# Performance work log

Measured on AMD Instinct MI355X. Metric: run time of the kernel, lower is better.

The kernel has to match this reference:

```python
import jax, jax.numpy as jnp
import numpy as np

B, C, L = 16, 128, 2048


def setup_inputs() -> dict:
    key = jax.random.key(0)
    ks = jax.random.split(key, 7)
    s = 1.0 / np.sqrt(C)  # torch Conv1d default init scale
    x = jax.random.normal(ks[0], (B, C, L), dtype=jnp.float32)
    W1 = jax.random.uniform(ks[1], (C, C), jnp.float32, -s, s)
    b1 = jax.random.uniform(ks[2], (C,), jnp.float32, -s, s)
    W2 = jax.random.uniform(ks[3], (C, C), jnp.float32, -s, s)
    b2 = jax.random.uniform(ks[4], (C,), jnp.float32, -s, s)
    W3 = jax.random.uniform(ks[5], (C, C), jnp.float32, -s, s)
    b3 = jax.random.uniform(ks[6], (C,), jnp.float32, -s, s)
    return {"x": x, "W1": W1, "b1": b1, "W2": W2, "b2": b2, "W3": W3, "b3": b3}


def _conv1x1(x, W, b):
    # x: [B,C,L], W: [out,in] -> [B,out,L]
    return jnp.einsum('oc,bcl->bol', W, x) + b[None, :, None]


def reference(x, W1, b1, W2, b2, W3, b3):
    q = _conv1x1(x, W1, b1).transpose(0, 2, 1)  # [B,L,C]
    k = _conv1x1(x, W2, b2).transpose(0, 2, 1)  # [B,L,C]
    v = _conv1x1(x, W3, b3).transpose(0, 2, 1)  # [B,L,C]
    attn = jnp.einsum('bic,bjc->bij', q, k)     # [B,L,L]
    attn = jax.nn.softmax(attn, axis=-1)
    out = jnp.einsum('bij,bjc->bic', attn, v)   # [B,L,C]
    return out.transpose(0, 2, 1)               # [B,C,L]
```

## Files before the change

### kernel.cpp

```cpp
#include <hip/hip_runtime.h>
#include <hip/hip_bf16.h>
#include <stdint.h>

#define B_ 16
#define C_ 128
#define L_ 2048
#define LOG2E 1.4426950408889634f

typedef __attribute__((ext_vector_type(8))) short bf16x8;
typedef __attribute__((ext_vector_type(4))) float f32x4;
typedef __attribute__((ext_vector_type(16))) float f32x16;
typedef __attribute__((ext_vector_type(4))) unsigned int u32x4;

typedef __attribute__((address_space(3))) unsigned int lds_u32_t;
typedef const __attribute__((address_space(1))) unsigned int gbl_u32_t;

__device__ __forceinline__ void gload_lds16(const void* g, void* l) {
  __builtin_amdgcn_global_load_lds((gbl_u32_t*)g,
                                   (lds_u32_t*)(unsigned long long)l, 16, 0, 0);
}

__device__ __forceinline__ unsigned short f2bf(float x) {
  union { float f; unsigned u; } v; v.f = x;
  unsigned u = v.u;
  u += 0x7fffu + ((u >> 16) & 1u);
  return (unsigned short)(u >> 16);
}

__device__ __forceinline__ unsigned pk2(float a, float b) {
  return (unsigned)f2bf(a) | ((unsigned)f2bf(b) << 16);
}

__device__ __forceinline__ unsigned cvtpk_bf16(float lo, float hi_) {
  unsigned r;
  asm("v_cvt_pk_bf16_f32 %0, %1, %2" : "=v"(r) : "v"(lo), "v"(hi_));
  return r;
}

__device__ __forceinline__ float max3f(float a, float b, float c) {
  float r;
  asm("v_max3_f32 %0, %1, %2, %3" : "=v"(r) : "v"(a), "v"(b), "v"(c));
  return r;
}

__device__ __forceinline__ f32x16 z16() {
  f32x16 v;
#pragma unroll
  for (int i = 0; i < 16; ++i) v[i] = 0.f;
  return v;
}

__device__ __forceinline__ float tmax16(const f32x16& v) {
  float m0 = max3f(v[0], v[1], v[2]);
  float m1 = max3f(v[3], v[4], v[5]);
  float m2_ = max3f(v[6], v[7], v[8]);
  float m3 = max3f(v[9], v[10], v[11]);
  float m4 = max3f(v[12], v[13], v[14]);
  float a = max3f(m0, m1, m2_);
  float b = max3f(m3, m4, v[15]);
  return fmaxf(a, b);
}

__device__ __forceinline__ float tsum16(const f32x16& v) {
  float a0 = v[0] + v[1],  a1 = v[2] + v[3];
  float a2 = v[4] + v[5],  a3 = v[6] + v[7];
  float a4 = v[8] + v[9],  a5 = v[10] + v[11];
  float a6 = v[12] + v[13], a7 = v[14] + v[15];
  float b0 = a0 + a1, b1 = a2 + a3, b2 = a4 + a5, b3 = a6 + a7;
  return (b0 + b1) + (b2 + b3);
}

__global__ __launch_bounds__(256, 2) void proj_kernel(
    const float* __restrict__ x,
    const float* __restrict__ W1, const float* __restrict__ b1,
    const float* __restrict__ W2, const float* __restrict__ b2,
    const float* __restrict__ W3, const float* __restrict__ b3,
    unsigned short* __restrict__ Qo, unsigned short* __restrict__ Ko,
    unsigned short* __restrict__ Vt)
{
  __shared__ unsigned short Xt[64][136];
  __shared__ unsigned short Wl[128][136];

  const int b  = blockIdx.x & 15;
  const int lt = blockIdx.x >> 4;
  const int l0 = lt * 64;
  const int tid = threadIdx.x;
  const int w = tid >> 6, lane = tid & 63, li = lane & 15, lg = lane >> 4;

  for (int it = 0; it < 8; ++it) {
    int idx = tid + it * 256;
    int c = idx >> 4, f4 = idx & 15;
    const float4 vv = *(const float4*)(x + (size_t)(b * C_ + c) * L_ + l0 + f4 * 4);
    Xt[f4 * 4 + 0][c] = f2bf(vv.x);
    Xt[f4 * 4 + 1][c] = f2bf(vv.y);
    Xt[f4 * 4 + 2][c] = f2bf(vv.z);
    Xt[f4 * 4 + 3][c] = f2bf(vv.w);
  }

  auto stageW = [&](const float* W) {
    for (int it = 0; it < 16; ++it) {
      int idx = tid + it * 256;
      int o = idx >> 5, f4 = idx & 31;
      const float4 vv = *(const float4*)(W + (size_t)o * C_ + f4 * 4);
      unsigned short* p = &Wl[o][f4 * 4];
      p[0] = f2bf(vv.x); p[1] = f2bf(vv.y); p[2] = f2bf(vv.z); p[3] = f2bf(vv.w);
    }
  };

  auto computePhase = [&](const float* bias, unsigned short* Out, int mode, float sc) {
    f32x4 acc[8];
#pragma unroll
    for (int ni = 0; ni < 8; ++ni) acc[ni] = (f32x4){0.f, 0.f, 0.f, 0.f};
    bf16x8 af[4];
#pragma unroll
    for (int kk = 0; kk < 4; ++kk)
      af[kk] = *(const bf16x8*)&Xt[w * 16 + li][lg * 8 + kk * 32];
#pragma unroll
    for (int kk = 0; kk < 4; ++kk) {
#pragma unroll
      for (int ni = 0; ni < 8; ++ni) {
        bf16x8 bf = *(const bf16x8*)&Wl[ni * 16 + li][lg * 8 + kk * 32];
        acc[ni] = __builtin_amdgcn_mfma_f32_16x16x32_bf16(af[kk], bf, acc[ni], 0, 0, 0);
      }
    }
    if (mode == 0) {
#pragma unroll
      for (int ni = 0; ni < 8; ++ni) {
        float bv = bias[ni * 16 + li];
#pragma unroll
        for (int r = 0; r < 4; ++r) {
          int lrow = l0 + w * 16 + lg * 4 + r;
          Out[(size_t)(b * L_ + lrow) * C_ + ni * 16 + li] = f2bf((acc[ni][r] + bv) * sc);
        }
      }
    } else {
#pragma unroll
      for (int ni = 0; ni < 8; ++ni) {
        float bv = bias[ni * 16 + li];
        int o = ni * 16 + li;
        unsigned long long pw =
            (unsigned long long)pk2(acc[ni][0] + bv, acc[ni][1] + bv) |
            ((unsigned long long)pk2(acc[ni][2] + bv, acc[ni][3] + bv) << 32);
        *(unsigned long long*)(Out + (size_t)(b * C_ + o) * L_ + l0 + w * 16 + lg * 4) = pw;
      }
    }
  };

  stageW(W1);
  __syncthreads();
  computePhase(b1, Qo, 0, LOG2E);
  __syncthreads();
  stageW(W2);
  __syncthreads();
  computePhase(b2, Ko, 0, 1.0f);
  __syncthreads();
  stageW(W3);
  __syncthreads();
  computePhase(b3, Vt, 1, 1.0f);
}

__global__ __launch_bounds__(256, 2) void attn_kernel(
    const unsigned short* __restrict__ Q,
    const unsigned short* __restrict__ K,
    const unsigned short* __restrict__ Vt,
    float* __restrict__ out)
{
  __shared__ char smem[65536 + 1024];

  const int b  = blockIdx.x & 15;
  const int qt = blockIdx.x >> 4;
  const int tid = threadIdx.x;
  const int w = tid >> 6, lane = tid & 63;
  const int q32 = lane & 31, hi = lane >> 5;
  const int qg = (w >> 1) & 1, jh = w & 1;
  const int qrow = qt * 64 + qg * 32 + q32;
  const size_t bLC = (size_t)b * L_ * C_;

  bf16x8 qf[8];
  {
    const unsigned short* qp = Q + bLC + (size_t)qrow * C_ + hi * 8;
#pragma unroll
    for (int kt = 0; kt < 8; ++kt) qf[kt] = *(const bf16x8*)(qp + kt * 16);
  }

  f32x16 oacc[4];
#pragma unroll
  for (int i = 0; i < 4; ++i) oacc[i] = z16();
  float m2 = -3e38f, lrun = 0.f;

  const char* kgb = (const char*)(K + bLC);
  const char* vgb = (const char*)(Vt + bLC);

  auto stage = [&](int sel, int t) {
    if (w < 2) {
      const char* ktb = kgb + (size_t)t * (64 * 256);
      char* dst = smem + sel * 16384 + w * 8192;
#pragma unroll
      for (int i2 = 0; i2 < 8; ++i2) {
        int d = w * 8192 + i2 * 1024 + lane * 16;
        int row = d >> 8, cb = d & 255;
        gload_lds16(ktb + row * 256 + (cb ^ ((row & 15) << 4)), dst + i2 * 1024);
      }
    } else {
      const char* vt0 = vgb + (size_t)t * 128;
      char* dst = smem + 32768 + sel * 16384 + (w - 2) * 8192;
#pragma unroll
      for (int i2 = 0; i2 < 8; ++i2) {
        int d = (w - 2) * 8192 + i2 * 1024 + lane * 16;
        int rc = d >> 7, cv = d & 127;
        gload_lds16(vt0 + (size_t)rc * (L_ * 2) + (cv ^ ((rc & 7) << 4)), dst + i2 * 1024);
      }
    }
  };

  stage(0, 0);
  __syncthreads();

  int cur = 0;
  for (int t = 0; t < 32; ++t) {
    if (t + 1 < 32) stage(cur ^ 1, t + 1);

    const char* kb = smem + cur * 16384;
    const int krow = jh * 32 + q32;
    const int kro  = krow << 8, ksw = (krow & 15) << 4;
    f32x16 s = z16();
    __builtin_amdgcn_s_setprio(1);
#pragma unroll
    for (int kt2 = 0; kt2 < 8; ++kt2) {
      bf16x8 kf = *(const bf16x8*)(kb + kro + ((kt2 * 32 + hi * 16) ^ ksw));
      s = __builtin_amdgcn_mfma_f32_32x32x16_bf16(kf, qf[kt2], s, 0, 0, 0);
    }
    __builtin_amdgcn_s_setprio(0);

    float pm = tmax16(s);
    pm = fmaxf(pm, __shfl_xor(pm, 32));
    if (!__all(pm - m2 <= 8.f)) {
      float mn = fmaxf(m2, pm);
      float al = exp2f(m2 - mn);
      lrun *= al;
#pragma unroll
      for (int ct = 0; ct < 4; ++ct) oacc[ct] = oacc[ct] * al;
      m2 = mn;
    }
#pragma unroll
    for (int r = 0; r < 16; ++r) s[r] = exp2f(s[r] - m2);
    float ps = tsum16(s);
    ps += __shfl_xor(ps, 32);
    lrun += ps;

    bf16x8 pf[2];
#pragma unroll
    for (int kj = 0; kj < 2; ++kj) {
      const int base = kj * 8;
      unsigned wl0 = cvtpk_bf16(s[base + 0], s[base + 1]);
      unsigned wl1 = cvtpk_bf16(s[base + 2], s[base + 3]);
      unsigned wh0 = cvtpk_bf16(s[base + 4], s[base + 5]);
      unsigned wh1 = cvtpk_bf16(s[base + 6], s[base + 7]);
      unsigned snd0 = hi ? wl0 : wh0;
      unsigned snd1 = hi ? wl1 : wh1;
      unsigned rcv0 = (unsigned)__shfl_xor((int)snd0, 32);
      unsigned rcv1 = (unsigned)__shfl_xor((int)snd1, 32);
      unsigned w0 = hi ? rcv0 : wl0;
      unsigned w1 = hi ? rcv1 : wl1;
      unsigned w2 = hi ? wh0 : rcv0;
      unsigned w3 = hi ? wh1 : rcv1;
      u32x4 pw = {w0, w1, w2, w3};
      pf[kj] = *reinterpret_cast<bf16x8*>(&pw);
    }

    const char* vb = smem + 32768 + cur * 16384;
    __builtin_amdgcn_s_setprio(1);
#pragma unroll
    for (int kj = 0; kj < 2; ++kj) {
      const int kjg = jh * 2 + kj;
#pragma unroll
      for (int ct = 0; ct < 4; ++ct) {
        int rowc = ct * 32 + q32;
        bf16x8 vf = *(const bf16x8*)(vb + (rowc << 7) +
                                     ((kjg * 32 + hi * 16) ^ ((rowc & 7) << 4)));
        oacc[ct] = __builtin_amdgcn_mfma_f32_32x32x16_bf16(vf, pf[kj], oacc[ct], 0, 0, 0);
      }
    }
    __builtin_amdgcn_s_setprio(0);

    __syncthreads();
    cur ^= 1;
  }

  float* mlb = (float*)(smem + 65536);
  if (hi == 0) {
    mlb[(w * 32 + q32) * 2 + 0] = m2;
    mlb[(w * 32 + q32) * 2 + 1] = lrun;
  }
  __syncthreads();
  const float mB = mlb[((w ^ 1) * 32 + q32) * 2 + 0];
  const float lB = mlb[((w ^ 1) * 32 + q32) * 2 + 1];
  const float mstar = fmaxf(m2, mB);
  const float aown  = exp2f(m2 - mstar);
  float* scrb = (float*)smem + (size_t)(qg * 64 + lane) * 33;
  float* ob = out + (size_t)b * C_ * L_ + qrow;
  float inv = 0.f;
  if (jh == 0) {
    const float aB = exp2f(mB - mstar);
    inv = 1.0f / (lrun * aown + lB * aB);
  }
  __syncthreads();
  if (jh == 1) {
#pragma unroll
    for (int r = 0; r < 16; ++r) {
      scrb[r]      = oacc[0][r] * aown;
      scrb[16 + r] = oacc[1][r] * aown;
    }
  }
  __syncthreads();
  if (jh == 0) {
#pragma unroll
    for (int ct = 0; ct < 2; ++ct)
#pragma unroll
      for (int r = 0; r < 16; ++r) {
        float v = oacc[ct][r] * aown + scrb[ct * 16 + r];
        int c = ct * 32 + (r & 3) + 8 * (r >> 2) + 4 * hi;
        ob[(size_t)c * L_] = v * inv;
      }
  }
  __syncthreads();
  if (jh == 1) {
#pragma unroll
    for (int r = 0; r < 16; ++r) {
      scrb[r]      = oacc[2][r] * aown;
      scrb[16 + r] = oacc[3][r] * aown;
    }
  }
  __syncthreads();
  if (jh == 0) {
#pragma unroll
    for (int ct = 0; ct < 2; ++ct)
#pragma unroll
      for (int r = 0; r < 16; ++r) {
        float v = oacc[2 + ct][r] * aown + scrb[ct * 16 + r];
        int c = (2 + ct) * 32 + (r & 3) + 8 * (r >> 2) + 4 * hi;
        ob[(size_t)c * L_] = v * inv;
      }
  }
}

extern "C" void kernel_launch(void* const* d_in, const int* in_sizes, int n_in,
                              void* d_out, int out_size, void* d_ws, size_t ws_size,
                              hipStream_t stream) {
  (void)in_sizes; (void)n_in; (void)out_size; (void)ws_size;
  const float* x  = (const float*)d_in[0];
  const float* W1 = (const float*)d_in[1];
  const float* b1 = (const float*)d_in[2];
  const float* W2 = (const float*)d_in[3];
  const float* b2 = (const float*)d_in[4];
  const float* W3 = (const float*)d_in[5];
  const float* b3 = (const float*)d_in[6];

  unsigned short* Q  = (unsigned short*)d_ws;
  unsigned short* K  = Q + (size_t)B_ * L_ * C_;
  unsigned short* Vt = K + (size_t)B_ * L_ * C_;

  proj_kernel<<<512, 256, 0, stream>>>(x, W1, b1, W2, b2, W3, b3, Q, K, Vt);
  attn_kernel<<<512, 256, 0, stream>>>(Q, K, Vt, (float*)d_out);
}
```

Measured before the change: 77.74 us.

## Pipeline K/V staging with partial vmcnt waits and precomputed LDS offsets

Restructures the attention main loop so the next tile's global-to-LDS loads are issued before waiting only on the previous tile's loads (vmcnt(8)), rather than a full __syncthreads that drains all outstanding loads. Global source and LDS read offsets are precomputed into registers, and the loop is unrolled by two so the buffer parity is a compile-time constant. Explicit s_barrier plus lgkmcnt waits and sched_barriers replace __syncthreads to control ordering. This adds register pressure from the offset arrays and relies on the hand-written waitcnt counts being correct.

```diff
diff --git a/kernel.cpp b/kernel.cpp
--- a/kernel.cpp
+++ b/kernel.cpp
@@ -165,7 +165,7 @@
     const unsigned short* __restrict__ Vt,
     float* __restrict__ out)
 {
-  __shared__ char smem[65536 + 1024];
+  __shared__ __align__(16) char smem[66560];
 
   const int b  = blockIdx.x & 15;
   const int qt = blockIdx.x >> 4;
@@ -188,47 +188,65 @@
   for (int i = 0; i < 4; ++i) oacc[i] = z16();
   float m2 = -3e38f, lrun = 0.f;
 
-  const char* kgb = (const char*)(K + bLC);
-  const char* vgb = (const char*)(Vt + bLC);
-
-  auto stage = [&](int sel, int t) {
-    if (w < 2) {
-      const char* ktb = kgb + (size_t)t * (64 * 256);
-      char* dst = smem + sel * 16384 + w * 8192;
-#pragma unroll
-      for (int i2 = 0; i2 < 8; ++i2) {
-        int d = w * 8192 + i2 * 1024 + lane * 16;
-        int row = d >> 8, cb = d & 255;
-        gload_lds16(ktb + row * 256 + (cb ^ ((row & 15) << 4)), dst + i2 * 1024);
-      }
-    } else {
-      const char* vt0 = vgb + (size_t)t * 128;
-      char* dst = smem + 32768 + sel * 16384 + (w - 2) * 8192;
-#pragma unroll
-      for (int i2 = 0; i2 < 8; ++i2) {
-        int d = (w - 2) * 8192 + i2 * 1024 + lane * 16;
-        int rc = d >> 7, cv = d & 127;
-        gload_lds16(vt0 + (size_t)rc * (L_ * 2) + (cv ^ ((rc & 7) << 4)), dst + i2 * 1024);
-      }
-    }
+  const int krow = jh * 32 + q32;
+  int kvo[8];
+#pragma unroll
+  for (int kt = 0; kt < 8; ++kt)
+    kvo[kt] = (krow << 8) + ((kt * 32 + hi * 16) ^ ((krow & 15) << 4));
+  int vvo[8];
+#pragma unroll
+  for (int kj = 0; kj < 2; ++kj)
+#pragma unroll
+    for (int ct = 0; ct < 4; ++ct) {
+      int rowc = ct * 32 + q32;
+      vvo[kj * 4 + ct] = (rowc << 7) + (((jh * 2 + kj) * 32 + hi * 16) ^ ((rowc & 7) << 4));
+    }
+
+  int soff[8];
+  const char* sp;
+  int dbase, sadv;
+  if (w < 2) {
+    sp = (const char*)(K + bLC);
+    dbase = w * 8192; sadv = 16384;
+#pragma unroll
+    for (int i2 = 0; i2 < 8; ++i2) {
+      int d = w * 8192 + i2 * 1024 + lane * 16;
+      int row = d >> 8, cb = d & 255;
+      soff[i2] = row * 256 + (cb ^ ((row & 15) << 4));
+    }
+  } else {
+    sp = (const char*)(Vt + bLC);
+    dbase = 32768 + (w - 2) * 8192; sadv = 128;
+#pragma unroll
+    for (int i2 = 0; i2 < 8; ++i2) {
+      int d = (w - 2) * 8192 + i2 * 1024 + lane * 16;
+      int rc = d >> 7, cv = d & 127;
+      soff[i2] = rc * 4096 + (cv ^ ((rc & 7) << 4));
+    }
+  }
+
+  auto stage_next = [&](int curx) {
+#pragma unroll
+    for (int i2 = 0; i2 < 8; ++i2)
+      gload_lds16(sp + soff[i2], &smem[dbase + (curx ^ 1) * 16384 + i2 * 1024]);
+    sp += sadv;
   };
 
-  stage(0, 0);
-  __syncthreads();
-
-  int cur = 0;
-  for (int t = 0; t < 32; ++t) {
-    if (t + 1 < 32) stage(cur ^ 1, t + 1);
-
-    const char* kb = smem + cur * 16384;
-    const int krow = jh * 32 + q32;
-    const int kro  = krow << 8, ksw = (krow & 15) << 4;
+  auto body = [&](int cur, int vmN, int do_stage) {
+    if (do_stage) stage_next(cur);
+    __builtin_amdgcn_sched_barrier(0);
+    if (vmN == 8) asm volatile("s_waitcnt vmcnt(8)" ::: "memory");
+    else          asm volatile("s_waitcnt vmcnt(0)" ::: "memory");
+    __builtin_amdgcn_s_barrier();
+    __builtin_amdgcn_sched_barrier(0);
+
+    const int KO = cur ? 16384 : 0;
     f32x16 s = z16();
     __builtin_amdgcn_s_setprio(1);
 #pragma unroll
-    for (int kt2 = 0; kt2 < 8; ++kt2) {
-      bf16x8 kf = *(const bf16x8*)(kb + kro + ((kt2 * 32 + hi * 16) ^ ksw));
-      s = __builtin_amdgcn_mfma_f32_32x32x16_bf16(kf, qf[kt2], s, 0, 0, 0);
+    for (int kt = 0; kt < 8; ++kt) {
+      bf16x8 kf = *(const bf16x8*)&smem[KO + kvo[kt]];
+      s = __builtin_amdgcn_mfma_f32_32x32x16_bf16(kf, qf[kt], s, 0, 0, 0);
     }
     __builtin_amdgcn_s_setprio(0);
 
@@ -268,24 +286,32 @@
       pf[kj] = *reinterpret_cast<bf16x8*>(&pw);
     }
 
-    const char* vb = smem + 32768 + cur * 16384;
+    const int VO = 32768 + KO;
     __builtin_amdgcn_s_setprio(1);
 #pragma unroll
-    for (int kj = 0; kj < 2; ++kj) {
-      const int kjg = jh * 2 + kj;
+    for (int kj = 0; kj < 2; ++kj)
 #pragma unroll
       for (int ct = 0; ct < 4; ++ct) {
-        int rowc = ct * 32 + q32;
-        bf16x8 vf = *(const bf16x8*)(vb + (rowc << 7) +
-                                     ((kjg * 32 + hi * 16) ^ ((rowc & 7) << 4)));
+        bf16x8 vf = *(const bf16x8*)&smem[VO + vvo[kj * 4 + ct]];
         oacc[ct] = __builtin_amdgcn_mfma_f32_32x32x16_bf16(vf, pf[kj], oacc[ct], 0, 0, 0);
       }
-    }
     __builtin_amdgcn_s_setprio(0);
 
-    __syncthreads();
-    cur ^= 1;
-  }
+    __builtin_amdgcn_sched_barrier(0);
+    asm volatile("s_waitcnt lgkmcnt(0)" ::: "memory");
+    __builtin_amdgcn_s_barrier();
+    __builtin_amdgcn_sched_barrier(0);
+  };
+
+  stage_next(1);
+  __builtin_amdgcn_sched_barrier(0);
+
+  for (int tt = 0; tt < 15; ++tt) {
+    body(0, 8, 1);
+    body(1, 8, 1);
+  }
+  body(0, 8, 1);
+  body(1, 0, 0);
 
   float* mlb = (float*)(smem + 65536);
   if (hi == 0) {
```

Measured after the change: 75.92 us. 2.3% less time.
